# Kernel optimization log

Measured on AMD Instinct MI355X. Metric: run time of the kernel, lower is better.

Reference implementation:

```python
import jax, jax.numpy as jnp
import numpy as np

H = 16      # num_heads
DK = 128    # head_dim_qk
DV = 128    # head_dim_v
HID = 2048  # hidden_size
KS = 4      # conv kernel size


def _causal_dwconv(x, w, b):
    # x: [B, T, C], w: [C, KS], b: [C] -- depthwise causal conv (torch pads KS-1 then slices [:T])
    xc = jnp.transpose(x, (0, 2, 1))  # [B, C, T]
    out = jax.lax.conv_general_dilated(
        xc, w[:, None, :], window_strides=(1,), padding=[(KS - 1, 0)],
        feature_group_count=xc.shape[1], dimension_numbers=('NCH', 'OIH', 'NCH'))
    out = out + b[None, :, None]
    return jnp.transpose(out, (0, 2, 1))


def setup_inputs() -> dict:
    key = jax.random.key(0)
    ks = jax.random.split(key, 16)
    s = 0.02
    inp = {
        'x':   jax.random.normal(ks[0], (4, 2048, HID), jnp.float32),
        'Wq':  jax.random.normal(ks[1], (HID, H * DK), jnp.float32) * s,
        'Wk':  jax.random.normal(ks[2], (HID, H * DK), jnp.float32) * s,
        'Wv':  jax.random.normal(ks[3], (HID, H * DV), jnp.float32) * s,
        'Wa':  jax.random.normal(ks[4], (HID, H), jnp.float32) * s,
        'ba':  jnp.zeros((H,), jnp.float32),
        'Wb':  jax.random.normal(ks[5], (HID, H), jnp.float32) * s,
        'bb':  jnp.zeros((H,), jnp.float32),
        'Wg':  jax.random.normal(ks[6], (HID, H * DV), jnp.float32) * s,
        'Wo':  jax.random.normal(ks[7], (H * DV, HID), jnp.float32) * s,
        'qcw': jax.random.normal(ks[8], (H * DK, KS), jnp.float32) * 0.3,
        'qcb': jnp.zeros((H * DK,), jnp.float32),
        'kcw': jax.random.normal(ks[9], (H * DK, KS), jnp.float32) * 0.3,
        'kcb': jnp.zeros((H * DK,), jnp.float32),
        'vcw': jax.random.normal(ks[10], (H * DV, KS), jnp.float32) * 0.3,
        'vcb': jnp.zeros((H * DV,), jnp.float32),
        'ln_w': jnp.ones((DV,), jnp.float32),
        'ln_b': jnp.zeros((DV,), jnp.float32),
    }
    return inp


def _forward(x, Wq, Wk, Wv, Wa, ba, Wb, bb, Wg, Wo, qcw, qcb, kcw, kcb, vcw, vcb, ln_w, ln_b):
    B, T, _ = x.shape
    q = jax.nn.silu(_causal_dwconv(x @ Wq, qcw, qcb))
    k = jax.nn.silu(_causal_dwconv(x @ Wk, kcw, kcb))
    v = jax.nn.silu(_causal_dwconv(x @ Wv, vcw, vcb))
    q = q.reshape(B, T, H, DK)
    k = k.reshape(B, T, H, DK) * (DK ** -0.5)
    v = v.reshape(B, T, H, DV)
    alpha = jax.nn.sigmoid(x @ Wa + ba)  # [B, T, H]
    beta = jax.nn.sigmoid(x @ Wb + bb)   # [B, T, H]

    # time-major for scan
    qT = jnp.transpose(q, (1, 0, 2, 3))
    kT = jnp.transpose(k, (1, 0, 2, 3))
    vT = jnp.transpose(v, (1, 0, 2, 3))
    aT = jnp.transpose(alpha, (1, 0, 2))
    bT = jnp.transpose(beta, (1, 0, 2))

    def step(S, inps):
        qt, kt, vt, at, bt = inps
        Sk = jnp.einsum('bhvk,bhk->bhv', S, kt)            # S @ k
        err = Sk - vt
        S = at[..., None, None] * S - bt[..., None, None] * (err[..., None] * kt[:, :, None, :])
        ot = jnp.einsum('bhvk,bhk->bhv', S, qt)            # output uses NEW state
        return S, ot

    S0 = jnp.zeros((B, H, DV, DK), x.dtype)
    _, oT = jax.lax.scan(step, S0, (qT, kT, vT, aT, bT))    # [T, B, H, DV]
    o = jnp.transpose(oT, (1, 0, 2, 3))                      # [B, T, H, DV]

    # LayerNorm over head_dim_v (eps=1e-5)
    mu = jnp.mean(o, axis=-1, keepdims=True)
    var = jnp.mean(jnp.square(o - mu), axis=-1, keepdims=True)
    o = (o - mu) * jax.lax.rsqrt(var + 1e-5) * ln_w + ln_b

    g = jax.nn.sigmoid(x @ Wg).reshape(B, T, H, DV)
    o = (o * g).reshape(B, T, H * DV)
    return o @ Wo


def reference(x, Wq, Wk, Wv, Wa, ba, Wb, bb, Wg, Wo, qcw, qcb, kcw, kcb, vcw, vcb, ln_w, ln_b):
    return _forward(x, Wq, Wk, Wv, Wa, ba, Wb, bb, Wg, Wo, qcw, qcb, kcw, kcb, vcw, vcb, ln_w, ln_b)
```

## Files before the change

### kernel.cpp

```cpp
#include <hip/hip_runtime.h>
#include <stdint.h>

#define H_   16
#define DK_  128
#define DV_  128
#define HID_ 2048
#define KS_  4
#define B_   4
#define T_   2048
#define BT_  (B_*T_)
#define QKVC (3*HID_)
#define C_   32
#define RS_  32
#define NC_  (T_/C_)

typedef unsigned short u16;
typedef short  bf16x8 __attribute__((ext_vector_type(8)));
typedef u16    u16x8  __attribute__((ext_vector_type(8)));
typedef u16    u16x4  __attribute__((ext_vector_type(4)));
typedef float  f32x4  __attribute__((ext_vector_type(4)));

__device__ __forceinline__ float b2f(u16 u){
  union { unsigned int i; float f; } v; v.i = ((unsigned int)u) << 16; return v.f;
}
__device__ __forceinline__ u16 f2b(float f){
  unsigned int x = __float_as_uint(f);
  unsigned int r = (x + 0x7FFFu + ((x >> 16) & 1u)) >> 16;
  return (u16)r;
}
__device__ __forceinline__ float sigm(float x){ return 1.0f / (1.0f + __expf(-x)); }

#define MFMA16(a,b,c) __builtin_amdgcn_mfma_f32_16x16x32_bf16((a),(b),(c),0,0,0)

__global__ __launch_bounds__(256) void cvt_x_k(const f32x4* __restrict__ src,
                                               u16x4* __restrict__ dst, int n4)
{
  int i0 = blockIdx.x * 256 + threadIdx.x;
  int stride = gridDim.x * 256;
  for (int i = i0; i < n4; i += stride) {
    f32x4 v = src[i];
    u16x4 r; r[0] = f2b(v[0]); r[1] = f2b(v[1]); r[2] = f2b(v[2]); r[3] = f2b(v[3]);
    dst[i] = r;
  }
}

__global__ __launch_bounds__(256) void cvt_small_k(
    const float* __restrict__ qcw, const float* __restrict__ kcw, const float* __restrict__ vcw,
    const float* __restrict__ qcb, const float* __restrict__ kcb, const float* __restrict__ vcb,
    const float* __restrict__ ba,  const float* __restrict__ bb,
    const float* __restrict__ lnw, const float* __restrict__ lnb,
    u16* __restrict__ canon)
{
  int i = blockIdx.x * 256 + threadIdx.x;
  if (i >= 31008) return;
  float v;
  if (i < 24576) {
    const float* s = (i < 8192) ? qcw : (i < 16384) ? kcw : vcw;
    v = s[i & 8191];
  } else if (i < 30720) {
    int j = i - 24576;
    const float* s = (j < 2048) ? qcb : (j < 4096) ? kcb : vcb;
    v = s[j & 2047];
  } else if (i < 30752) {
    int j = i - 30720;
    v = (j < 16) ? ba[j] : bb[j - 16];
  } else {
    int j = i - 30752;
    v = (j < 128) ? lnw[j] : lnb[j - 128];
  }
  canon[i] = f2b(v);
}

__global__ __launch_bounds__(256) void transpose_b(const float* __restrict__ s0,
                                                   const float* __restrict__ s1,
                                                   const float* __restrict__ s2,
                                                   u16* __restrict__ dst,
                                                   int R, int C)
{
  int z = blockIdx.z;
  const float* src = (z == 0) ? s0 : (z == 1) ? s1 : s2;
  u16* d = dst + (size_t)z * R * C;
  __shared__ u16 t[32][33];
  int bx = blockIdx.x * 32;
  int by = blockIdx.y * 32;
  int lx = threadIdx.x & 31, ly = threadIdx.x >> 5;
  #pragma unroll
  for (int i = 0; i < 4; ++i) {
    int r = by + ly + i * 8, c = bx + lx;
    if (r < R && c < C) t[ly + i * 8][lx] = f2b(src[(size_t)r * C + c]);
  }
  __syncthreads();
  #pragma unroll
  for (int i = 0; i < 4; ++i) {
    int r = bx + ly + i * 8;
    int c = by + lx;
    if (r < C && c < R) d[(size_t)r * R + c] = t[lx][ly + i * 8];
  }
}

#define BM 128
#define BN 128
#define BK 32

__device__ __forceinline__ void gload_lds16(const void* gp, void* lp){
  __builtin_amdgcn_global_load_lds(
      (const __attribute__((address_space(1))) void*)gp,
      (__attribute__((address_space(3))) void*)lp, 16, 0, 0);
}

__global__ __launch_bounds__(256) void gemm_bt(const u16* __restrict__ A, int lda,
                                               const u16* __restrict__ Bt, int ldb,
                                               void* __restrict__ C, int ldc,
                                               int K, int out_f32)
{
  __shared__ u16 lsA[BM * BK];
  __shared__ u16 lsB[BN * BK];
  int tid = threadIdx.x, wave = tid >> 6, lane = tid & 63;
  int m0 = blockIdx.y * BM, n0 = blockIdx.x * BN;
  int wm = (wave >> 1) * 64, wn = (wave & 1) * 64;
  int srow = lane >> 2;
  int skel = (lane & 3) * 8;
  int quad = lane >> 4, l16 = lane & 15;

  f32x4 acc[4][4];
  #pragma unroll
  for (int mi = 0; mi < 4; ++mi)
    #pragma unroll
    for (int ni = 0; ni < 4; ++ni)
      #pragma unroll
      for (int r = 0; r < 4; ++r) acc[mi][ni][r] = 0.0f;

  for (int k0 = 0; k0 < K; k0 += BK) {
    __syncthreads();
    #pragma unroll
    for (int i = 0; i < 2; ++i) {
      int row = wave * 32 + i * 16 + srow;
      gload_lds16(A  + (size_t)(m0 + row) * lda + k0 + skel,
                  lsA + (wave * 2048 + i * 1024) / 2);
      gload_lds16(Bt + (size_t)(n0 + row) * ldb + k0 + skel,
                  lsB + (wave * 2048 + i * 1024) / 2);
    }
    __syncthreads();

    const bf16x8* fA = (const bf16x8*)lsA;
    const bf16x8* fB = (const bf16x8*)lsB;
    bf16x8 af[4], bg[4];
    #pragma unroll
    for (int mi = 0; mi < 4; ++mi) af[mi] = fA[(wm + mi * 16 + l16) * 4 + quad];
    #pragma unroll
    for (int ni = 0; ni < 4; ++ni) bg[ni] = fB[(wn + ni * 16 + l16) * 4 + quad];
    #pragma unroll
    for (int mi = 0; mi < 4; ++mi)
      #pragma unroll
      for (int ni = 0; ni < 4; ++ni)
        acc[mi][ni] = MFMA16(af[mi], bg[ni], acc[mi][ni]);
  }

  #pragma unroll
  for (int mi = 0; mi < 4; ++mi)
    #pragma unroll
    for (int ni = 0; ni < 4; ++ni)
      #pragma unroll
      for (int r = 0; r < 4; ++r) {
        int m = m0 + wm + mi * 16 + quad * 4 + r;
        int n = n0 + wn + ni * 16 + l16;
        if (out_f32) ((float*)C)[(size_t)m * ldc + n] = acc[mi][ni][r];
        else         ((u16*)C)[(size_t)m * ldc + n] = f2b(acc[mi][ni][r]);
      }
}

__global__ __launch_bounds__(256) void ab_k(const u16* __restrict__ x,
                                            const u16* __restrict__ WabT,
                                            const u16* __restrict__ ba,
                                            const u16* __restrict__ bb,
                                            float* __restrict__ ab)
{
  int j = threadIdx.x & 31, rl = threadIdx.x >> 5;
  int row = blockIdx.x * 8 + rl;
  const u16x8* xr = (const u16x8*)(x + (size_t)row * HID_);
  const u16x8* wr = (const u16x8*)(WabT + (size_t)j * HID_);
  float acc = 0.f;
  for (int k = 0; k < HID_ / 8; ++k) {
    u16x8 xv = xr[k], wv = wr[k];
    #pragma unroll
    for (int i = 0; i < 8; ++i) acc += b2f(xv[i]) * b2f(wv[i]);
  }
  float bias = (j < 16) ? b2f(ba[j]) : b2f(bb[j - 16]);
  float sg = sigm(acc + bias);
  if (j < 16) ab[(size_t)row * 16 + j] = sg;
  else        ab[(size_t)BT_ * 16 + (size_t)row * 16 + (j - 16)] = sg;
}

__global__ __launch_bounds__(256) void conv_silu_k(const u16* __restrict__ in,
                                                   const u16* __restrict__ cwv,
                                                   const u16* __restrict__ cbv,
                                                   u16* __restrict__ out)
{
  int idx  = blockIdx.x * 256 + threadIdx.x;
  int col8 = idx % (QKVC / 8);
  int t    = idx / (QKVC / 8);
  int col  = col8 * 8;
  int s = col >> 11;

  u16 wl[32];
  #pragma unroll
  for (int i = 0; i < 4; ++i)
    *(u16x8*)(wl + i * 8) = *(const u16x8*)(cwv + (size_t)col * KS_ + i * 8);
  u16x8 bv = *(const u16x8*)(cbv + col);

  float acc[8];
  #pragma unroll
  for (int j = 0; j < 8; ++j) acc[j] = b2f(bv[j]);

  #pragma unroll
  for (int tap = 0; tap < KS_; ++tap) {
    int tt = t - 3 + tap;
    if (tt >= 0) {
      u16x8 xv = *(const u16x8*)(in + (size_t)tt * QKVC + col);
      #pragma unroll
      for (int j = 0; j < 8; ++j) acc[j] = fmaf(b2f(xv[j]), b2f(wl[j * 4 + tap]), acc[j]);
    }
  }
  float scale = (s == 1) ? 0.08838834764831845f : 1.0f;
  u16x8 rv;
  #pragma unroll
  for (int j = 0; j < 8; ++j) {
    float a = acc[j];
    rv[j] = f2b(a * sigm(a) * scale);
  }
  *(u16x8*)(out + (size_t)t * QKVC + col) = rv;
}

__global__ __launch_bounds__(256) void chunk_scan_k(const u16* __restrict__ qkv,
                                                    const float* __restrict__ ab,
                                                    u16* __restrict__ o)
{
  __shared__ __align__(16) char smem[64512];
  u16 (*Kim)[136] = (u16(*)[136])(smem);
  u16 (*Qim)[136] = (u16(*)[136])(smem + 8704);
  u16 (*Sh)[136]  = (u16(*)[136])(smem + 17408);
  u16 (*Sl)[136]  = (u16(*)[136])(smem + 26112);
  u16 (*KT)[40]   = (u16(*)[40])(smem + 34816);
  u16 (*Vim)[32]  = (u16(*)[32])(smem + 45056);
  float (*KK)[33] = (float(*)[33])(smem + 47104);
  float (*KQ)[33] = (float(*)[33])(smem + 51328);
  float (*SK0)[33]= (float(*)[33])(smem + 55552);
  float (*SQ0)[33]= (float(*)[33])(smem + 59776);
  float (*PL4)[4] = (float(*)[4])(smem + 64000);

  int bid = blockIdx.x;
  int chain = bid & 63, rblk = bid >> 6;
  int b = chain >> 4, h = chain & 15;
  int tid = threadIdx.x, wv = tid >> 6, lane = tid & 63;
  int l16 = lane & 15, quad = lane >> 4, r32 = lane & 31;

  float (*Uw)[33] = (float(*)[33])(smem + 8704 + wv * 4224);

  const u16* kbase = qkv + (size_t)b * T_ * QKVC + HID_ + h * DK_;
  const u16* qbase = qkv + (size_t)b * T_ * QKVC + h * DK_;
  const u16* vbase = qkv + (size_t)b * T_ * QKVC + 2 * HID_ + h * DV_ + rblk * RS_;
  const float* abase = ab + (size_t)b * T_ * 16 + h;
  const float* bbase = abase + (size_t)BT_ * 16;
  u16* obase = o + (size_t)b * T_ * 2048 + h * DV_ + rblk * RS_;

  f32x4 st[2][2];
  #pragma unroll
  for (int rt = 0; rt < 2; ++rt)
    #pragma unroll
    for (int ct = 0; ct < 2; ++ct)
      #pragma unroll
      for (int r = 0; r < 4; ++r) st[rt][ct][r] = 0.f;

  int jb = tid - 64;
  u16x8 stg[6];
  float avp = 0.f;

  auto LD = [&](int c) {
    int t0 = c * C_;
    if (wv == 0) {
      avp = (lane < 32) ? abase[(size_t)(t0 + lane) * 16]
                        : bbase[(size_t)(t0 + lane - 32) * 16];
    } else {
      #pragma unroll
      for (int it = 0; it < 6; ++it) {
        int j = jb + it * 192;
        if (j < 512) {
          int t = j >> 4, g = j & 15;
          stg[it] = *(const u16x8*)(kbase + (size_t)(t0 + t) * QKVC + g * 8);
        } else if (j < 1024) {
          int j2 = j - 512, t = j2 >> 4, g = j2 & 15;
          stg[it] = *(const u16x8*)(qbase + (size_t)(t0 + t) * QKVC + g * 8);
        } else {
          int j2 = j - 1024, t = j2 >> 2, rg = j2 & 3;
          stg[it] = *(const u16x8*)(vbase + (size_t)(t0 + t) * QKVC + rg * 8);
        }
      }
    }
  };

  LD(0);

  for (int c = 0; c < NC_; ++c) {
    int t0 = c * C_;

    #pragma unroll
    for (int rt = 0; rt < 2; ++rt)
      #pragma unroll
      for (int ct = 0; ct < 2; ++ct)
        #pragma unroll
        for (int r = 0; r < 4; ++r) {
          float s = st[rt][ct][r];
          u16 hi = f2b(s);
          float lo = s - b2f(hi);
          int row = rt * 16 + quad * 4 + r;
          int col = wv * 32 + ct * 16 + l16;
          Sh[row][col] = hi;
          Sl[row][col] = f2b(lo);
        }

    if (wv == 0) {
      float av = avp;
      float p = av;
      #pragma unroll
      for (int d = 1; d < 32; d <<= 1) {
        float up = __shfl_up(p, d);
        if (lane >= d && lane < 32) p *= up;
      }
      float pm1 = __shfl_up(p, 1);
      float bt = __shfl(av, lane + 32);
      if (lane < 32) {
        if (lane == 0) pm1 = 1.f;
        f32x4 g;
        g[0] = bt * pm1; g[1] = bt; g[2] = 1.0f / p; g[3] = p;
        *(f32x4*)PL4[lane] = g;
      }
    } else {
      #pragma unroll
      for (int it = 0; it < 6; ++it) {
        int j = jb + it * 192;
        if (j < 512) {
          int t = j >> 4, g = j & 15;
          *(u16x8*)&Kim[t][g * 8] = stg[it];
          int blk = ((t >> 3) ^ (g & 3)) << 3;
          int tl = t & 7;
          #pragma unroll
          for (int e = 0; e < 8; ++e)
            KT[g * 8 + e][blk + tl] = stg[it][e];
        } else if (j < 1024) {
          int j2 = j - 512, t = j2 >> 4, g = j2 & 15;
          *(u16x8*)&Qim[t][g * 8] = stg[it];
        } else {
          int j2 = j - 1024, t = j2 >> 2, rg = j2 & 3;
          *(u16x8*)&Vim[t][rg * 8] = stg[it];
        }
      }
    }
    if (c + 1 < NC_) LD(c + 1);
    __syncthreads();

    {
      auto dotKK = [&](int mt, int nt) {
        f32x4 acc = {0.f,0.f,0.f,0.f};
        #pragma unroll
        for (int ks = 0; ks < 4; ++ks) {
          bf16x8 A = *(const bf16x8*)&Kim[mt * 16 + l16][ks * 32 + quad * 8];
          bf16x8 B = *(const bf16x8*)&Kim[nt * 16 + l16][ks * 32 + quad * 8];
          acc = MFMA16(A, B, acc);
        }
        #pragma unroll
        for (int r = 0; r < 4; ++r) KK[mt * 16 + quad * 4 + r][nt * 16 + l16] = acc[r];
      };
      auto dotKQ = [&](int mt, int nt) {
        f32x4 acc = {0.f,0.f,0.f,0.f};
        #pragma unroll
        for (int ks = 0; ks < 4; ++ks) {
          bf16x8 A = *(const bf16x8*)&Qim[mt * 16 + l16][ks * 32 + quad * 8];
          bf16x8 B = *(const bf16x8*)&Kim[nt * 16 + l16][ks * 32 + quad * 8];
          acc = MFMA16(A, B, acc);
        }
        #pragma unroll
        for (int r = 0; r < 4; ++r) KQ[mt * 16 + quad * 4 + r][nt * 16 + l16] = acc[r];
      };
      auto dotS = [&](const u16 (*Aarr)[136], int tt, int rr, float (*OUT)[33]) {
        f32x4 acc = {0.f,0.f,0.f,0.f};
        #pragma unroll
        for (int ks = 0; ks < 4; ++ks) {
          bf16x8 A  = *(const bf16x8*)&Aarr[tt * 16 + l16][ks * 32 + quad * 8];
          bf16x8 Bh = *(const bf16x8*)&Sh[rr * 16 + l16][ks * 32 + quad * 8];
          bf16x8 Bl = *(const bf16x8*)&Sl[rr * 16 + l16][ks * 32 + quad * 8];
          acc = MFMA16(A, Bh, acc);
          acc = MFMA16(A, Bl, acc);
        }
        #pragma unroll
        for (int r = 0; r < 4; ++r) OUT[tt * 16 + quad * 4 + r][rr * 16 + l16] = acc[r];
      };
      if (wv == 0)      { dotS(Kim, 0, 0, SK0); dotS(Kim, 1, 0, SK0); dotKK(0, 0); dotKK(1, 0); }
      else if (wv == 1) { dotS(Kim, 0, 1, SK0); dotS(Kim, 1, 1, SK0); dotKK(1, 1); dotKQ(0, 0); }
      else if (wv == 2) { dotS(Qim, 0, 0, SQ0); dotS(Qim, 1, 0, SQ0); dotKQ(1, 0); }
      else              { dotS(Qim, 0, 1, SQ0); dotS(Qim, 1, 1, SQ0); dotKQ(1, 1); }
    }
    __syncthreads();

    {
      float ub[C_];
      #pragma unroll
      for (int t = 0; t < C_; ++t) {
        f32x4 g = *(const f32x4*)PL4[t];
        float u = g[0] * SK0[t][r32] - g[1] * b2f(Vim[t][r32]);
        float acc = 0.f;
        #pragma unroll
        for (int i = 0; i < t; ++i) acc = fmaf(KK[t][i], ub[i], acc);
        u = fmaf(-g[0], acc, u);
        if (lane < 32) Uw[t][lane] = u;
        ub[t] = g[2] * u;
      }

      float PL31 = PL4[31][3];

      #pragma unroll
      for (int rt = 0; rt < 2; ++rt) {
        union { u16x8 u; bf16x8 b; } ah, al;
        #pragma unroll
        for (int e = 0; e < 8; ++e) {
          int i = quad * 8 + e;
          float uv = Uw[i][rt * 16 + l16];
          float ucv = -PL31 * PL4[i][2] * uv;
          u16 hh = f2b(ucv);
          ah.u[e] = hh; al.u[e] = f2b(ucv - b2f(hh));
        }
        #pragma unroll
        for (int ct = 0; ct < 2; ++ct) {
          int col = wv * 32 + ct * 16 + l16;
          bf16x8 Bk = *(const bf16x8*)&KT[col][(quad ^ ((col >> 3) & 3)) << 3];
          f32x4 cacc;
          #pragma unroll
          for (int r = 0; r < 4; ++r) cacc[r] = PL31 * st[rt][ct][r];
          cacc = MFMA16(ah.b, Bk, cacc);
          cacc = MFMA16(al.b, Bk, cacc);
          st[rt][ct] = cacc;
        }
      }

      int mt = wv >> 1, nt = wv & 1;
      union { u16x8 u; bf16x8 b; } gh, gl, uth, utl;
      int trow = mt * 16 + l16;
      float Pt = PL4[trow][3];
      #pragma unroll
      for (int e = 0; e < 8; ++e) {
        int i = quad * 8 + e;
        float uv = Uw[i][nt * 16 + l16];
        u16 h1 = f2b(uv);
        uth.u[e] = h1; utl.u[e] = f2b(uv - b2f(h1));
        float gv = (i <= trow) ? (-Pt * PL4[i][2] * KQ[trow][i]) : 0.f;
        u16 h2 = f2b(gv);
        gh.u[e] = h2; gl.u[e] = f2b(gv - b2f(h2));
      }
      f32x4 oacc;
      #pragma unroll
      for (int r = 0; r < 4; ++r) {
        int t = mt * 16 + quad * 4 + r;
        oacc[r] = PL4[t][3] * SQ0[t][nt * 16 + l16];
      }
      oacc = MFMA16(gh.b, uth.b, oacc);
      oacc = MFMA16(gh.b, utl.b, oacc);
      oacc = MFMA16(gl.b, uth.b, oacc);
      #pragma unroll
      for (int r = 0; r < 4; ++r) {
        int t = mt * 16 + quad * 4 + r;
        obase[(size_t)(t0 + t) * 2048 + nt * 16 + l16] = f2b(oacc[r]);
      }
    }
    __syncthreads();
  }
}

__global__ __launch_bounds__(256) void ln_gate_k(const u16* __restrict__ o_raw,
                                                 const u16* __restrict__ g,
                                                 const u16* __restrict__ lnw,
                                                 const u16* __restrict__ lnb,
                                                 u16* __restrict__ o_ln)
{
  int gid = blockIdx.x * 4 + (threadIdx.x >> 6);
  int lane = threadIdx.x & 63;
  int row = gid >> 4, h = gid & 15;
  size_t ofs = (size_t)row * 2048 + h * 128 + lane * 2;
  unsigned int e2 = *(const unsigned int*)(o_raw + ofs);
  float ex = b2f((u16)(e2 & 0xffff)), ey = b2f((u16)(e2 >> 16));
  float s = ex + ey, ss = ex * ex + ey * ey;
  #pragma unroll
  for (int m = 1; m < 64; m <<= 1) { s += __shfl_xor(s, m); ss += __shfl_xor(ss, m); }
  float mean = s * (1.f / 128.f);
  float var  = ss * (1.f / 128.f) - mean * mean;
  float rstd = rsqrtf(fmaxf(var, 0.f) + 1e-5f);
  float w0 = b2f(lnw[lane * 2]), w1 = b2f(lnw[lane * 2 + 1]);
  float b0 = b2f(lnb[lane * 2]), b1 = b2f(lnb[lane * 2 + 1]);
  unsigned int g2 = *(const unsigned int*)(g + ofs);
  float g0 = sigm(b2f((u16)(g2 & 0xffff))), g1 = sigm(b2f((u16)(g2 >> 16)));
  float r0 = ((ex - mean) * rstd * w0 + b0) * g0;
  float r1 = ((ey - mean) * rstd * w1 + b1) * g1;
  *(unsigned int*)(o_ln + ofs) = (unsigned int)f2b(r0) | ((unsigned int)f2b(r1) << 16);
}

extern "C" void kernel_launch(void* const* d_in, const int* in_sizes, int n_in,
                              void* d_out, int out_size, void* d_ws, size_t ws_size,
                              hipStream_t stream)
{
  const float* x   = (const float*)d_in[0];
  const float* Wq  = (const float*)d_in[1];
  const float* Wk  = (const float*)d_in[2];
  const float* Wv  = (const float*)d_in[3];
  const float* Wa  = (const float*)d_in[4];
  const float* ba  = (const float*)d_in[5];
  const float* Wb  = (const float*)d_in[6];
  const float* bb  = (const float*)d_in[7];
  const float* Wg  = (const float*)d_in[8];
  const float* Wo  = (const float*)d_in[9];
  const float* qcw = (const float*)d_in[10];
  const float* qcb = (const float*)d_in[11];
  const float* kcw = (const float*)d_in[12];
  const float* kcb = (const float*)d_in[13];
  const float* vcw = (const float*)d_in[14];
  const float* vcb = (const float*)d_in[15];
  const float* lnw = (const float*)d_in[16];
  const float* lnb = (const float*)d_in[17];
  (void)in_sizes; (void)n_in; (void)out_size;

  char* ws = (char*)d_ws;
  size_t off = 0;
  auto alloc = [&](size_t bytes) -> void* {
    void* p = ws + off; off += (bytes + 255) & ~(size_t)255; return p;
  };
  u16* WT    = (u16*)alloc((size_t)3 * HID_ * HID_ * 2);
  u16* WabT  = (u16*)alloc((size_t)32 * HID_ * 2);
  u16* xc    = (u16*)alloc((size_t)BT_ * HID_ * 2);
  u16* canon = (u16*)alloc((size_t)31008 * 2);
  u16* preC  = (u16*)alloc((size_t)BT_ * HID_ * 2 * 2);
  u16* post  = (u16*)alloc((size_t)BT_ * QKVC * 2);
  float* abuf = (float*)alloc((size_t)2 * BT_ * 16 * 4);
  if (off > ws_size) return;

  u16* cw_c  = canon;
  u16* cb_c  = canon + 24576;
  u16* ba_c  = canon + 30720;
  u16* bb_c  = canon + 30736;
  u16* lnw_c = canon + 30752;
  u16* lnb_c = canon + 30880;

  u16* o_raw = preC;
  u16* g_raw = post;
  u16* o_ln  = post + (size_t)BT_ * HID_;
  u16* WTg   = WT;

  dim3 tb(256);

  cvt_x_k<<<dim3(4096), tb, 0, stream>>>((const f32x4*)x, (u16x4*)xc, BT_ * HID_ / 4);
  cvt_small_k<<<dim3(122), tb, 0, stream>>>(qcw, kcw, vcw, qcb, kcb, vcb, ba, bb, lnw, lnb, canon);

  transpose_b<<<dim3(64, 64, 3), tb, 0, stream>>>(Wq, Wk, Wv, WT, HID_, HID_);
  transpose_b<<<dim3(1, 64, 2), tb, 0, stream>>>(Wa, Wb, Wb, WabT, HID_, 16);

  for (int b = 0; b < B_; ++b) {
    const u16* xb = xc + (size_t)b * T_ * HID_;
    gemm_bt<<<dim3(QKVC / BN, T_ / BM), tb, 0, stream>>>(xb, HID_, WT, HID_, preC, QKVC, HID_, 0);
    conv_silu_k<<<dim3(T_ * (QKVC / 8) / 256), tb, 0, stream>>>(
        preC, cw_c, cb_c, post + (size_t)b * T_ * QKVC);
  }

  transpose_b<<<dim3(64, 64, 2), tb, 0, stream>>>(Wg, Wo, Wo, WTg, HID_, HID_);

  ab_k<<<dim3(BT_ / 8), tb, 0, stream>>>(xc, WabT, ba_c, bb_c, abuf);

  chunk_scan_k<<<dim3(256), tb, 0, stream>>>(post, abuf, o_raw);

  gemm_bt<<<dim3(HID_ / BN, BT_ / BM), tb, 0, stream>>>(xc, HID_, WTg, HID_, g_raw, HID_, HID_, 0);

  ln_gate_k<<<dim3(BT_ * H_ / 4), tb, 0, stream>>>(o_raw, g_raw, lnw_c, lnb_c, o_ln);

  gemm_bt<<<dim3(HID_ / BN, BT_ / BM), tb, 0, stream>>>(o_ln, HID_,
      WT + (size_t)HID_ * HID_, HID_, d_out, HID_, HID_, 1);
}
```

Before: 1.408 ms.

## Replace GEMM with double-buffered 256x256 tile kernel and batch QKV projection

Replaces the 128x128x32 single-buffered GEMM with a 512-thread 256x256x64 kernel. It double-buffers LDS, prefetching the next K tile with direct global-to-LDS loads while the current tile is computed, and remaps workgroups with a grid swizzle for better cache locality. When the workspace is large enough, the QKV projection runs as one GEMM over all batches instead of four per-batch launches. The bigger tile raises data reuse per load, but it uses about 128KB of LDS per block, which limits occupancy to one block per CU. It also requires a larger preC buffer.

```diff
diff --git a/kernel.cpp b/kernel.cpp
--- a/kernel.cpp
+++ b/kernel.cpp
@@ -98,72 +98,82 @@
   }
 }
 
-#define BM 128
-#define BN 128
-#define BK 32
-
 __device__ __forceinline__ void gload_lds16(const void* gp, void* lp){
   __builtin_amdgcn_global_load_lds(
       (const __attribute__((address_space(1))) void*)gp,
       (__attribute__((address_space(3))) void*)lp, 16, 0, 0);
 }
 
-__global__ __launch_bounds__(256) void gemm_bt(const u16* __restrict__ A, int lda,
-                                               const u16* __restrict__ Bt, int ldb,
-                                               void* __restrict__ C, int ldc,
-                                               int K, int out_f32)
-{
-  __shared__ u16 lsA[BM * BK];
-  __shared__ u16 lsB[BN * BK];
-  int tid = threadIdx.x, wave = tid >> 6, lane = tid & 63;
-  int m0 = blockIdx.y * BM, n0 = blockIdx.x * BN;
-  int wm = (wave >> 1) * 64, wn = (wave & 1) * 64;
-  int srow = lane >> 2;
-  int skel = (lane & 3) * 8;
-  int quad = lane >> 4, l16 = lane & 15;
-
-  f32x4 acc[4][4];
-  #pragma unroll
-  for (int mi = 0; mi < 4; ++mi)
+#define GBM 256
+#define GBN 256
+#define GBK 64
+
+__global__ __launch_bounds__(512, 2) void gemm256(const u16* __restrict__ A, int lda,
+                                                  const u16* __restrict__ Bt, int ldb,
+                                                  void* __restrict__ C, int ldc,
+                                                  int K, int out_f32)
+{
+  __shared__ u16 lsA[2][GBM * GBK];
+  __shared__ u16 lsB[2][GBN * GBK];
+  int tid = threadIdx.x, wid = tid >> 6, lane = tid & 63;
+  int l16 = lane & 15, quad = lane >> 4;
+  int wr = wid >> 2, wc = wid & 3;
+
+  int nbx = gridDim.x;
+  int nwg = nbx * gridDim.y;
+  int flat = blockIdx.y * nbx + blockIdx.x;
+  int swzid = ((nwg & 7) == 0) ? ((flat & 7) * (nwg >> 3) + (flat >> 3)) : flat;
+  int m0 = (swzid / nbx) * GBM;
+  int n0 = (swzid % nbx) * GBN;
+
+  f32x4 acc[8][4] = {};
+
+  auto STAGE = [&](int t, int bi){
+    int k0 = t * GBK;
+    #pragma unroll
+    for (int ld = 0; ld < 4; ++ld) {
+      int slot = ld * 512 + tid;
+      int row = slot >> 3, cg = slot & 7;
+      int lofs = (ld * 512 + wid * 64) * 8;
+      gload_lds16(A  + (size_t)(m0 + row) * lda + k0 + cg * 8, &lsA[bi][lofs]);
+      gload_lds16(Bt + (size_t)(n0 + row) * ldb + k0 + cg * 8, &lsB[bi][lofs]);
+    }
+  };
+
+  STAGE(0, 0);
+  __syncthreads();
+
+  int NT = K / GBK;
+  for (int t = 0; t < NT; ++t) {
+    int bi = t & 1;
+    if (t + 1 < NT) STAGE(t + 1, bi ^ 1);
+    const u16* pA = lsA[bi];
+    const u16* pB = lsB[bi];
+    #pragma unroll
+    for (int ks = 0; ks < 2; ++ks) {
+      bf16x8 bfr[4];
+      #pragma unroll
+      for (int ni = 0; ni < 4; ++ni)
+        bfr[ni] = *(const bf16x8*)&pB[(wc * 64 + ni * 16 + l16) * GBK + ks * 32 + quad * 8];
+      #pragma unroll
+      for (int mi = 0; mi < 8; ++mi) {
+        bf16x8 af = *(const bf16x8*)&pA[(wr * 128 + mi * 16 + l16) * GBK + ks * 32 + quad * 8];
+        #pragma unroll
+        for (int ni = 0; ni < 4; ++ni)
+          acc[mi][ni] = MFMA16(af, bfr[ni], acc[mi][ni]);
+      }
+    }
+    __syncthreads();
+  }
+
+  #pragma unroll
+  for (int mi = 0; mi < 8; ++mi)
     #pragma unroll
     for (int ni = 0; ni < 4; ++ni)
       #pragma unroll
-      for (int r = 0; r < 4; ++r) acc[mi][ni][r] = 0.0f;
-
-  for (int k0 = 0; k0 < K; k0 += BK) {
-    __syncthreads();
-    #pragma unroll
-    for (int i = 0; i < 2; ++i) {
-      int row = wave * 32 + i * 16 + srow;
-      gload_lds16(A  + (size_t)(m0 + row) * lda + k0 + skel,
-                  lsA + (wave * 2048 + i * 1024) / 2);
-      gload_lds16(Bt + (size_t)(n0 + row) * ldb + k0 + skel,
-                  lsB + (wave * 2048 + i * 1024) / 2);
-    }
-    __syncthreads();
-
-    const bf16x8* fA = (const bf16x8*)lsA;
-    const bf16x8* fB = (const bf16x8*)lsB;
-    bf16x8 af[4], bg[4];
-    #pragma unroll
-    for (int mi = 0; mi < 4; ++mi) af[mi] = fA[(wm + mi * 16 + l16) * 4 + quad];
-    #pragma unroll
-    for (int ni = 0; ni < 4; ++ni) bg[ni] = fB[(wn + ni * 16 + l16) * 4 + quad];
-    #pragma unroll
-    for (int mi = 0; mi < 4; ++mi)
-      #pragma unroll
-      for (int ni = 0; ni < 4; ++ni)
-        acc[mi][ni] = MFMA16(af[mi], bg[ni], acc[mi][ni]);
-  }
-
-  #pragma unroll
-  for (int mi = 0; mi < 4; ++mi)
-    #pragma unroll
-    for (int ni = 0; ni < 4; ++ni)
-      #pragma unroll
       for (int r = 0; r < 4; ++r) {
-        int m = m0 + wm + mi * 16 + quad * 4 + r;
-        int n = n0 + wn + ni * 16 + l16;
+        int m = m0 + wr * 128 + mi * 16 + quad * 4 + r;
+        int n = n0 + wc * 64 + ni * 16 + l16;
         if (out_f32) ((float*)C)[(size_t)m * ldc + n] = acc[mi][ni][r];
         else         ((u16*)C)[(size_t)m * ldc + n] = f2b(acc[mi][ni][r]);
       }
@@ -534,9 +544,15 @@
   u16* WabT  = (u16*)alloc((size_t)32 * HID_ * 2);
   u16* xc    = (u16*)alloc((size_t)BT_ * HID_ * 2);
   u16* canon = (u16*)alloc((size_t)31008 * 2);
-  u16* preC  = (u16*)alloc((size_t)BT_ * HID_ * 2 * 2);
   u16* post  = (u16*)alloc((size_t)BT_ * QKVC * 2);
   float* abuf = (float*)alloc((size_t)2 * BT_ * 16 * 4);
+  size_t base_off = off;
+
+  size_t fused_need = base_off + (((size_t)BT_ * QKVC * 2 + 255) & ~(size_t)255);
+  int fused = (fused_need <= ws_size);
+  u16* preC;
+  if (fused) preC = (u16*)alloc((size_t)BT_ * QKVC * 2);
+  else       preC = (u16*)alloc((size_t)BT_ * HID_ * 2 * 2);
   if (off > ws_size) return;
 
   u16* cw_c  = canon;
@@ -551,7 +567,7 @@
   u16* o_ln  = post + (size_t)BT_ * HID_;
   u16* WTg   = WT;
 
-  dim3 tb(256);
+  dim3 tb(256), tb5(512);
 
   cvt_x_k<<<dim3(4096), tb, 0, stream>>>((const f32x4*)x, (u16x4*)xc, BT_ * HID_ / 4);
   cvt_small_k<<<dim3(122), tb, 0, stream>>>(qcw, kcw, vcw, qcb, kcb, vcb, ba, bb, lnw, lnb, canon);
@@ -559,11 +575,18 @@
   transpose_b<<<dim3(64, 64, 3), tb, 0, stream>>>(Wq, Wk, Wv, WT, HID_, HID_);
   transpose_b<<<dim3(1, 64, 2), tb, 0, stream>>>(Wa, Wb, Wb, WabT, HID_, 16);
 
-  for (int b = 0; b < B_; ++b) {
-    const u16* xb = xc + (size_t)b * T_ * HID_;
-    gemm_bt<<<dim3(QKVC / BN, T_ / BM), tb, 0, stream>>>(xb, HID_, WT, HID_, preC, QKVC, HID_, 0);
-    conv_silu_k<<<dim3(T_ * (QKVC / 8) / 256), tb, 0, stream>>>(
-        preC, cw_c, cb_c, post + (size_t)b * T_ * QKVC);
+  if (fused) {
+    gemm256<<<dim3(QKVC / GBN, BT_ / GBM), tb5, 0, stream>>>(xc, HID_, WT, HID_, preC, QKVC, HID_, 0);
+    for (int b = 0; b < B_; ++b)
+      conv_silu_k<<<dim3(T_ * (QKVC / 8) / 256), tb, 0, stream>>>(
+          preC + (size_t)b * T_ * QKVC, cw_c, cb_c, post + (size_t)b * T_ * QKVC);
+  } else {
+    for (int b = 0; b < B_; ++b) {
+      const u16* xb = xc + (size_t)b * T_ * HID_;
+      gemm256<<<dim3(QKVC / GBN, T_ / GBM), tb5, 0, stream>>>(xb, HID_, WT, HID_, preC, QKVC, HID_, 0);
+      conv_silu_k<<<dim3(T_ * (QKVC / 8) / 256), tb, 0, stream>>>(
+          preC, cw_c, cb_c, post + (size_t)b * T_ * QKVC);
+    }
   }
 
   transpose_b<<<dim3(64, 64, 2), tb, 0, stream>>>(Wg, Wo, Wo, WTg, HID_, HID_);
@@ -572,10 +595,10 @@
 
   chunk_scan_k<<<dim3(256), tb, 0, stream>>>(post, abuf, o_raw);
 
-  gemm_bt<<<dim3(HID_ / BN, BT_ / BM), tb, 0, stream>>>(xc, HID_, WTg, HID_, g_raw, HID_, HID_, 0);
+  gemm256<<<dim3(HID_ / GBN, BT_ / GBM), tb5, 0, stream>>>(xc, HID_, WTg, HID_, g_raw, HID_, HID_, 0);
 
   ln_gate_k<<<dim3(BT_ * H_ / 4), tb, 0, stream>>>(o_raw, g_raw, lnw_c, lnb_c, o_ln);
 
-  gemm_bt<<<dim3(HID_ / BN, BT_ / BM), tb, 0, stream>>>(o_ln, HID_,
+  gemm256<<<dim3(HID_ / GBN, BT_ / GBM), tb5, 0, stream>>>(o_ln, HID_,
       WT + (size_t)HID_ * HID_, HID_, d_out, HID_, HID_, 1);
 }
```

Measured after the change: 1.312 ms. 6.8% less time.
